# Kernel tuning notes

Hardware: AMD Instinct MI355X
Metric: run time of the kernel (lower is better)

Reference implementation:

```python
import jax, jax.numpy as jnp
import numpy as np
from jax import lax

UP = 4          # upscale_factor (pixel_shuffle factor hardcoded to 4 in ReconBlock)
OUT_CH = UP * UP * 5 * 5  # 400
MID_CH = UP * 5           # 20


def setup_inputs() -> dict:
    key = jax.random.key(0)
    ks = jax.random.split(key, 5)
    B, A, H, W = 2, 5, 96, 96
    pic = jax.random.uniform(ks[0], (B, A, A, H, W), dtype=jnp.float32)
    w1 = jax.random.normal(ks[1], (OUT_CH, 1, 5, 5, 9, 9), dtype=jnp.float32) * 0.02
    b1 = jnp.zeros((OUT_CH,), jnp.float32)
    w2a = jax.random.normal(ks[2], (MID_CH, 1, 3, 3, 5, 5), dtype=jnp.float32) * 0.02
    b2a = jnp.zeros((MID_CH,), jnp.float32)
    w2b = jax.random.normal(ks[3], (OUT_CH, MID_CH, 3, 3, 5, 5), dtype=jnp.float32) * 0.02
    b2b = jnp.zeros((OUT_CH,), jnp.float32)
    return {"pic": pic, "w1": w1, "b1": b1, "w2a": w2a, "b2a": b2a,
            "w2b": w2b, "b2b": b2b}


def _conv4d(x, w):
    # x: [B, Cin, A1, A2, H, W], w: [Cout, Cin, k1, k2, k3, k4], VALID, stride 1
    return lax.conv_general_dilated(x, w, window_strides=(1, 1, 1, 1),
                                    padding='VALID')


def _bias(b):
    return b[None, :, None, None, None, None]


def reference(pic, w1, b1, w2a, b2a, w2b, b2b):
    B, A1, A2, H, W = pic.shape
    # Padder: pad H,W by 4 each side with value 0.5
    padded = jnp.full((B, A1, A2, H + 8, W + 8), 0.5, dtype=pic.dtype)
    padded = padded.at[:, :, :, 4:-4, 4:-4].set(pic)
    x = padded[:, None]  # [B,1,A1,A2,H+8,W+8]

    # DimBlock_1: single 4D conv (5,5,9,9); ReLU defined but never applied
    p1 = _conv4d(x, w1) + _bias(b1)              # [B,400,1,1,H,W]

    # DimBlock_2: two 4D convs (3,3,5,5) with ReLU
    buf = jax.nn.relu(_conv4d(x, w2a) + _bias(b2a))   # [B,20,3,3,H+4,W+4]
    p2 = jax.nn.relu(_conv4d(buf, w2b) + _bias(b2b))  # [B,400,1,1,H,W]

    # BottleNeck
    mid = (p1 + p2) / 2                           # [B,400,1,1,H,W]

    # ReconBlock: take angular position (0,0), pixel_shuffle(4), split 25 -> 5x5
    y = mid[:, :, 0, 0]                           # [B,400,H,W]
    Bc, C, Hh, Ww = y.shape
    r = 4
    y = y.reshape(Bc, 25, r, r, Hh, Ww)
    y = y.transpose(0, 1, 4, 2, 5, 3).reshape(Bc, 25, Hh * r, Ww * r)
    return y.reshape(Bc, 5, 5, Hh * r, Ww * r)
```

## Files before the change

### kernel.cpp

```cpp
#include <hip/hip_runtime.h>
#include <hip/hip_bf16.h>


typedef __attribute__((ext_vector_type(8))) unsigned short ushort8;
typedef __attribute__((ext_vector_type(8))) __bf16 bf16x8;
typedef __attribute__((ext_vector_type(4))) float f32x4;

#define NB 2
#define HSLOT 576
#define HBUF (4 * HSLOT * 8)
#define WST 14336
#define NWA (6 * 25 * 7 * 4 * 64 * 8)
#define NWB (81 * 7 * 4 * 64 * 8)

static __device__ __forceinline__ unsigned short f2bf(float f) {
    __hip_bfloat16 h = __float2bfloat16(f);
    return *reinterpret_cast<unsigned short*>(&h);
}
static __device__ __forceinline__ void gload16(const unsigned short* g, unsigned short* l) {
    __builtin_amdgcn_global_load_lds(
        (const __attribute__((address_space(1))) unsigned int*)(const void*)g,
        (__attribute__((address_space(3))) unsigned int*)(void*)l, 16, 0, 0);
}

#define MFMA16(A0, A1, A2, A3, B0, B1, B2, B3)                                          \
    {                                                                                   \
        __builtin_amdgcn_s_setprio(1);                                                  \
        acc[0][0] = __builtin_amdgcn_mfma_f32_16x16x32_bf16(A0, B0, acc[0][0], 0, 0, 0);\
        acc[0][1] = __builtin_amdgcn_mfma_f32_16x16x32_bf16(A0, B1, acc[0][1], 0, 0, 0);\
        acc[0][2] = __builtin_amdgcn_mfma_f32_16x16x32_bf16(A0, B2, acc[0][2], 0, 0, 0);\
        acc[0][3] = __builtin_amdgcn_mfma_f32_16x16x32_bf16(A0, B3, acc[0][3], 0, 0, 0);\
        acc[1][0] = __builtin_amdgcn_mfma_f32_16x16x32_bf16(A1, B0, acc[1][0], 0, 0, 0);\
        acc[1][1] = __builtin_amdgcn_mfma_f32_16x16x32_bf16(A1, B1, acc[1][1], 0, 0, 0);\
        acc[1][2] = __builtin_amdgcn_mfma_f32_16x16x32_bf16(A1, B2, acc[1][2], 0, 0, 0);\
        acc[1][3] = __builtin_amdgcn_mfma_f32_16x16x32_bf16(A1, B3, acc[1][3], 0, 0, 0);\
        acc[2][0] = __builtin_amdgcn_mfma_f32_16x16x32_bf16(A2, B0, acc[2][0], 0, 0, 0);\
        acc[2][1] = __builtin_amdgcn_mfma_f32_16x16x32_bf16(A2, B1, acc[2][1], 0, 0, 0);\
        acc[2][2] = __builtin_amdgcn_mfma_f32_16x16x32_bf16(A2, B2, acc[2][2], 0, 0, 0);\
        acc[2][3] = __builtin_amdgcn_mfma_f32_16x16x32_bf16(A2, B3, acc[2][3], 0, 0, 0);\
        acc[3][0] = __builtin_amdgcn_mfma_f32_16x16x32_bf16(A3, B0, acc[3][0], 0, 0, 0);\
        acc[3][1] = __builtin_amdgcn_mfma_f32_16x16x32_bf16(A3, B1, acc[3][1], 0, 0, 0);\
        acc[3][2] = __builtin_amdgcn_mfma_f32_16x16x32_bf16(A3, B2, acc[3][2], 0, 0, 0);\
        acc[3][3] = __builtin_amdgcn_mfma_f32_16x16x32_bf16(A3, B3, acc[3][3], 0, 0, 0);\
        __builtin_amdgcn_s_setprio(0);                                                  \
    }

__global__ __launch_bounds__(256) void pad_kernel(const float* __restrict__ pic,
                                                  unsigned short* __restrict__ Pn) {
    int idx = blockIdx.x * 256 + threadIdx.x;
    if (idx >= NB * 104 * 104) return;
    int x = idx % 104;
    int y = (idx / 104) % 104;
    int b = idx / (104 * 104);
    unsigned short vals[32];
    bool inter = (y >= 4 && y < 100 && x >= 4 && x < 100);
#pragma unroll
    for (int c = 0; c < 25; ++c) {
        float v = inter ? pic[((b * 25 + c) * 96 + (y - 4)) * 96 + (x - 4)] : 0.5f;
        vals[c] = f2bf(v);
    }
#pragma unroll
    for (int c = 25; c < 32; ++c) vals[c] = 0;
    ushort8* dst = (ushort8*)(Pn + idx * 32);
#pragma unroll
    for (int j = 0; j < 4; ++j) dst[j] = *(ushort8*)&vals[j * 8];
}

__global__ __launch_bounds__(256) void prep_w_kernel(const float* __restrict__ w2b,
                                                     const float* __restrict__ w1,
                                                     unsigned short* __restrict__ Wp) {
    int idx = blockIdx.x * 256 + threadIdx.x;
    if (idx < NWA) {
        int e = idx & 7, lane = (idx >> 3) & 63, n = (idx >> 9) & 3;
        int r = idx >> 11;
        int ocb = r % 7; r /= 7;
        int tap = r % 25; int cc = r / 25;
        int oc = ocb * 64 + n * 16 + (lane & 15);
        int k  = cc * 32 + (lane >> 4) * 8 + e;
        float v = 0.f;
        if (oc < 400 && k < 180) {
            int mc = k % 20, uv = k / 20;
            v = w2b[oc * 4500 + (mc * 9 + uv) * 25 + tap];
        }
        Wp[idx] = f2bf(v);
    } else {
        int kx = idx - NWA;
        if (kx >= NWB) return;
        int e = kx & 7, lane = (kx >> 3) & 63, n = (kx >> 9) & 3;
        int r = kx >> 11;
        int ocb = r % 7; int tp = r / 7;
        int dy, dx;
        if (tp < 45) { dy = tp / 5; dx = tp % 5; }
        else { int u = tp - 45; dy = u >> 2; dx = 5 + (u & 3); }
        int oc = ocb * 64 + n * 16 + (lane & 15);
        int c  = (lane >> 4) * 8 + e;
        float v = (oc < 400 && c < 25) ? w1[oc * 2025 + c * 81 + (dy * 9 + dx)] : 0.f;
        Wp[NWA + kx] = f2bf(v);
    }
}

__global__ __launch_bounds__(256) void conv2a_mfma_kernel(
    const unsigned short* __restrict__ Pn, const float* __restrict__ w2a,
    const float* __restrict__ b2a, unsigned short* __restrict__ Bn) {
    __shared__ __align__(16) unsigned short sWc[25 * 2048];
    __shared__ __align__(16) unsigned short sHalo[4 * 448 * 8];

    const int tid  = threadIdx.x;
    const int lane = tid & 63, w = tid >> 6;
    const int l15  = lane & 15, lhi = lane >> 4;
    const int gx0  = blockIdx.x;
    const int b    = gx0 / 52, t52 = gx0 % 52;
    const int ty0  = (t52 >> 2) * 8;
    const int tx0  = (t52 & 3) * 32;
    const int ocB  = blockIdx.y;

    {
        int oc = ocB * 64 + w * 16 + (lane & 15);
        int kb = (lane >> 4) * 8;
        int uv = oc / 20;
        int mc = oc - uv * 20;
        int u = uv / 3, v = uv - (uv / 3) * 3;
        const float* wb[8];
#pragma unroll
        for (int e = 0; e < 8; ++e) {
            int k  = kb + e;
            int c1 = k / 5, c2 = k - (k / 5) * 5;
            int da1 = c1 - u, da2 = c2 - v;
            bool valid = (oc < 180) && ((unsigned)da1 < 3u) && ((unsigned)da2 < 3u);
            wb[e] = valid ? (w2a + mc * 225 + (da1 * 3 + da2) * 25) : (const float*)0;
        }
#pragma unroll
        for (int tap = 0; tap < 25; ++tap) {
            unsigned short fr[8];
#pragma unroll
            for (int e = 0; e < 8; ++e) fr[e] = wb[e] ? f2bf(wb[e][tap]) : (unsigned short)0;
            *(ushort8*)&sWc[tap * 2048 + tid * 8] = *(ushort8*)fr;
        }
    }

    for (int L2 = 0; L2 < 7; ++L2) {
        int p = L2 * 64 + lane;
        if (p >= 432) p = 0;
        int hy = (p * 58255) >> 21, hx = p - hy * 36;
        int gy = ty0 + hy; gy = gy > 103 ? 103 : gy;
        int gx = tx0 + hx; gx = gx > 103 ? 103 : gx;
        gload16(Pn + ((size_t)((b * 104 + gy) * 104 + gx)) * 32 + w * 8,
                &sHalo[(w * 448 + L2 * 64) * 8]);
    }
    float bs[4];
#pragma unroll
    for (int n = 0; n < 4; ++n) {
        int oc = ocB * 64 + n * 16 + l15;
        bs[n] = (oc < 180) ? b2a[oc % 20] : 0.f;
    }
    __syncthreads();

    const unsigned short* hb = &sHalo[(lhi * 448 + w * 72 + l15) * 8];
    const unsigned short* wc = &sWc[lane * 8];

    f32x4 acc[4][4] = {};
    bf16x8 a0 = *(const bf16x8*)(hb), a1 = *(const bf16x8*)(hb + 128);
    bf16x8 a2 = *(const bf16x8*)(hb + 288), a3 = *(const bf16x8*)(hb + 416);
    bf16x8 c0 = *(const bf16x8*)(wc), c1 = *(const bf16x8*)(wc + 512);
    bf16x8 c2 = *(const bf16x8*)(wc + 1024), c3 = *(const bf16x8*)(wc + 1536);
    bf16x8 q0, q1, q2, q3, n0, n1, n2, n3;
#pragma unroll
    for (int t = 0; t < 25; ++t) {
        if (t < 24) {
            const int u = (((t + 1) / 5) * 36 + ((t + 1) % 5)) * 8;
            q0 = *(const bf16x8*)(hb + u);
            q1 = *(const bf16x8*)(hb + u + 128);
            q2 = *(const bf16x8*)(hb + u + 288);
            q3 = *(const bf16x8*)(hb + u + 416);
            const unsigned short* wn = wc + (t + 1) * 2048;
            n0 = *(const bf16x8*)(wn);
            n1 = *(const bf16x8*)(wn + 512);
            n2 = *(const bf16x8*)(wn + 1024);
            n3 = *(const bf16x8*)(wn + 1536);
        }
        MFMA16(a0, a1, a2, a3, c0, c1, c2, c3);
        if (t < 24) { a0 = q0; a1 = q1; a2 = q2; a3 = q3;
                      c0 = n0; c1 = n1; c2 = n2; c3 = n3; }
    }

#pragma unroll
    for (int n = 0; n < 4; ++n) {
        int oc = ocB * 64 + n * 16 + l15;
#pragma unroll
        for (int m = 0; m < 4; ++m) {
            int y = ty0 + w * 2 + (m >> 1);
            if (y >= 100) continue;
            int x0 = tx0 + (m & 1) * 16 + lhi * 4;
#pragma unroll
            for (int i = 0; i < 4; ++i) {
                int x = x0 + i;
                if (x >= 100) continue;
                Bn[((size_t)((b * 100 + y) * 100 + x)) * 192 + oc] =
                    f2bf(fmaxf(acc[m][n][i] + bs[n], 0.f));
            }
        }
    }
}

__global__ __launch_bounds__(256, 2) void conv_mfma_kernel(
    const unsigned short* __restrict__ Pn, const unsigned short* __restrict__ Bn,
    const unsigned short* __restrict__ Wp, const float* __restrict__ b1,
    const float* __restrict__ b2b, float* __restrict__ out) {
    __shared__ __align__(16) unsigned short sHalo[2 * HBUF];

    const int tid  = threadIdx.x;
    const int lane = tid & 63, w = tid >> 6;
    const int l15  = lane & 15, lhi = lane >> 4;
    const int ocB  = blockIdx.y;
    const int pb   = blockIdx.x;
    const int b    = pb / 36;
    const int t36  = pb % 36;
    const int ty0  = (t36 / 3) * 8;
    const int tx0  = (t36 % 3) * 32;

    const int vA = (lhi * HSLOT + w * 72 + l15) * 8;

    auto stageA = [&](int cc, int par) {
        unsigned short* dst0 = &sHalo[par * HBUF + w * HSLOT * 8];
        for (int L2 = 0; L2 < 7; ++L2) {
            int p = L2 * 64 + lane;
            if (p >= 432) p = 0;
            int hy = (p * 58255) >> 21, hx = p - hy * 36;
            gload16(Bn + ((size_t)((b * 100 + ty0 + hy) * 100 + tx0 + hx)) * 192 +
                        cc * 32 + w * 8,
                    dst0 + L2 * 512);
        }
    };
    auto stageB = [&](int seg, int par) {
        int cx = tx0 + (seg == 7 ? 5 : 0);
        unsigned short* dst0 = &sHalo[par * HBUF + w * HSLOT * 8];
        for (int L2 = 0; L2 < 9; ++L2) {
            int p = L2 * 64 + lane;
            int hy = (p * 58255) >> 21, hx = p - hy * 36;
            int gx = cx + hx;
            gx = gx > 103 ? 103 : gx;
            gload16(Pn + ((size_t)((b * 104 + ty0 + hy) * 104 + gx)) * 32 + w * 8,
                    dst0 + L2 * 512);
        }
    };

    float bb2[4], bb1[4];
#pragma unroll
    for (int n = 0; n < 4; ++n) {
        int oc  = ocB * 64 + n * 16 + l15;
        int occ = oc < 400 ? oc : 399;
        bb2[n] = b2b[occ];
        bb1[n] = b1[occ];
    }

    const unsigned short* wq = Wp + ocB * 2048 + lane * 8;
    bf16x8 c0 = *(const bf16x8*)(wq);
    bf16x8 c1 = *(const bf16x8*)(wq + 512);
    bf16x8 c2 = *(const bf16x8*)(wq + 1024);
    bf16x8 c3 = *(const bf16x8*)(wq + 1536);
    stageA(0, 0);
    __syncthreads();

    f32x4 acc[4][4] = {};
    bf16x8 a0, a1, a2, a3, q0, q1, q2, q3, n0, n1, n2, n3;

    for (int cc = 0; cc < 6; ++cc) {
        const unsigned short* hb = &sHalo[(cc & 1) * HBUF + vA];
        a0 = *(const bf16x8*)(hb);
        a1 = *(const bf16x8*)(hb + 128);
        a2 = *(const bf16x8*)(hb + 288);
        a3 = *(const bf16x8*)(hb + 416);
        if (cc < 5) stageA(cc + 1, (cc + 1) & 1);
        else        stageB(6, 0);
#pragma unroll
        for (int t = 0; t < 25; ++t) {
            wq += WST;
            n0 = *(const bf16x8*)(wq);
            n1 = *(const bf16x8*)(wq + 512);
            n2 = *(const bf16x8*)(wq + 1024);
            n3 = *(const bf16x8*)(wq + 1536);
            if (t < 24) {
                const int u = (((t + 1) / 5) * 36 + ((t + 1) % 5)) * 8;
                q0 = *(const bf16x8*)(hb + u);
                q1 = *(const bf16x8*)(hb + u + 128);
                q2 = *(const bf16x8*)(hb + u + 288);
                q3 = *(const bf16x8*)(hb + u + 416);
            }
            MFMA16(a0, a1, a2, a3, c0, c1, c2, c3);
            c0 = n0; c1 = n1; c2 = n2; c3 = n3;
            if (t < 24) { a0 = q0; a1 = q1; a2 = q2; a3 = q3; }
        }
        if (cc == 5) {
#pragma unroll
            for (int m = 0; m < 4; ++m)
#pragma unroll
                for (int n = 0; n < 4; ++n)
#pragma unroll
                    for (int i = 0; i < 4; ++i)
                        acc[m][n][i] = fmaxf(acc[m][n][i] + bb2[n], 0.f);
        }
        asm volatile("s_waitcnt vmcnt(4)" ::: "memory");
        asm volatile("s_barrier" ::: "memory");
    }

    {
        const unsigned short* hb = &sHalo[vA];
        a0 = *(const bf16x8*)(hb);
        a1 = *(const bf16x8*)(hb + 128);
        a2 = *(const bf16x8*)(hb + 288);
        a3 = *(const bf16x8*)(hb + 416);
        stageB(7, 1);
#pragma unroll
        for (int t = 0; t < 45; ++t) {
            wq += WST;
            n0 = *(const bf16x8*)(wq);
            n1 = *(const bf16x8*)(wq + 512);
            n2 = *(const bf16x8*)(wq + 1024);
            n3 = *(const bf16x8*)(wq + 1536);
            if (t < 44) {
                const int u = (((t + 1) / 5) * 36 + ((t + 1) % 5)) * 8;
                q0 = *(const bf16x8*)(hb + u);
                q1 = *(const bf16x8*)(hb + u + 128);
                q2 = *(const bf16x8*)(hb + u + 288);
                q3 = *(const bf16x8*)(hb + u + 416);
            }
            MFMA16(a0, a1, a2, a3, c0, c1, c2, c3);
            c0 = n0; c1 = n1; c2 = n2; c3 = n3;
            if (t < 44) { a0 = q0; a1 = q1; a2 = q2; a3 = q3; }
        }
        asm volatile("s_waitcnt vmcnt(4)" ::: "memory");
        asm volatile("s_barrier" ::: "memory");
    }

    {
        const unsigned short* hb = &sHalo[HBUF + vA];
        a0 = *(const bf16x8*)(hb);
        a1 = *(const bf16x8*)(hb + 128);
        a2 = *(const bf16x8*)(hb + 288);
        a3 = *(const bf16x8*)(hb + 416);
#pragma unroll
        for (int t = 0; t < 36; ++t) {
            if (t < 35) {
                wq += WST;
                n0 = *(const bf16x8*)(wq);
                n1 = *(const bf16x8*)(wq + 512);
                n2 = *(const bf16x8*)(wq + 1024);
                n3 = *(const bf16x8*)(wq + 1536);
                const int u = (((t + 1) / 4) * 36 + ((t + 1) % 4)) * 8;
                q0 = *(const bf16x8*)(hb + u);
                q1 = *(const bf16x8*)(hb + u + 128);
                q2 = *(const bf16x8*)(hb + u + 288);
                q3 = *(const bf16x8*)(hb + u + 416);
            }
            MFMA16(a0, a1, a2, a3, c0, c1, c2, c3);
            if (t < 35) { a0 = q0; a1 = q1; a2 = q2; a3 = q3;
                          c0 = n0; c1 = n1; c2 = n2; c3 = n3; }
        }
    }

#pragma unroll
    for (int n = 0; n < 4; ++n) {
        int oc = ocB * 64 + n * 16 + l15;
        if (oc >= 400) continue;
        float bv = bb1[n];
        int c25 = oc >> 4, r1 = (oc >> 2) & 3, r2 = oc & 3;
#pragma unroll
        for (int m = 0; m < 4; ++m) {
            int y  = ty0 + w * 2 + (m >> 1);
            int x0 = tx0 + (m & 1) * 16 + lhi * 4;
#pragma unroll
            for (int i = 0; i < 4; ++i) {
                out[((size_t)(b * 25 + c25) * 384 + y * 4 + r1) * 384 + (x0 + i) * 4 + r2] =
                    (acc[m][n][i] + bv) * 0.5f;
            }
        }
    }
}

extern "C" void kernel_launch(void* const* d_in, const int* in_sizes, int n_in,
                              void* d_out, int out_size, void* d_ws, size_t ws_size,
                              hipStream_t stream) {
    const float* pic = (const float*)d_in[0];
    const float* w1  = (const float*)d_in[1];
    const float* b1  = (const float*)d_in[2];
    const float* w2a = (const float*)d_in[3];
    const float* b2a = (const float*)d_in[4];
    const float* w2b = (const float*)d_in[5];
    const float* b2b = (const float*)d_in[6];
    float* out = (float*)d_out;

    char* ws = (char*)d_ws;
    unsigned short* Pn = (unsigned short*)(ws);
    unsigned short* Bn = (unsigned short*)(ws + 1384448);
    unsigned short* Wp = (unsigned short*)(ws + 9064448);

    pad_kernel<<<(NB * 104 * 104 + 255) / 256, 256, 0, stream>>>(pic, Pn);
    prep_w_kernel<<<(NWA + NWB + 255) / 256, 256, 0, stream>>>(w2b, w1, Wp);
    conv2a_mfma_kernel<<<dim3(104, 3), 256, 0, stream>>>(Pn, w2a, b2a, Bn);
    conv_mfma_kernel<<<dim3(72, 7), 256, 0, stream>>>(Pn, Bn, Wp, b1, b2b, out);
}
```

Baseline: 160.0 us.

## Split conv taps across wave pairs with LDS reduction and larger per-wave M tile

Restructures the main conv kernel so each wave computes an 8x4 MFMA tile (doubling the rows per wave) while pairs of waves split the K-loop taps in half, reducing partial sums through an LDS exchange buffer. This halves the weight-fragment loads per MFMA and increases reuse of B fragments. In exchange it drops double-buffered halo staging and software prefetch, adds full barriers between stages, and doubles accumulator registers, which may reduce occupancy. The weight prep kernel is also vectorised to write 8 bf16 values per thread.

```diff
diff --git a/kernel.cpp b/kernel.cpp
--- a/kernel.cpp
+++ b/kernel.cpp
@@ -8,7 +8,6 @@
 
 #define NB 2
 #define HSLOT 576
-#define HBUF (4 * HSLOT * 8)
 #define WST 14336
 #define NWA (6 * 25 * 7 * 4 * 64 * 8)
 #define NWB (81 * 7 * 4 * 64 * 8)
@@ -21,6 +20,72 @@
     __builtin_amdgcn_global_load_lds(
         (const __attribute__((address_space(1))) unsigned int*)(const void*)g,
         (__attribute__((address_space(3))) unsigned int*)(void*)l, 16, 0, 0);
+}
+
+__global__ __launch_bounds__(256) void pad_kernel(const float* __restrict__ pic,
+                                                  unsigned short* __restrict__ Pn) {
+    int idx = blockIdx.x * 256 + threadIdx.x;
+    if (idx >= NB * 104 * 104) return;
+    int x = idx % 104;
+    int y = (idx / 104) % 104;
+    int b = idx / (104 * 104);
+    unsigned short vals[32];
+    bool inter = (y >= 4 && y < 100 && x >= 4 && x < 100);
+#pragma unroll
+    for (int c = 0; c < 25; ++c) {
+        float v = inter ? pic[((b * 25 + c) * 96 + (y - 4)) * 96 + (x - 4)] : 0.5f;
+        vals[c] = f2bf(v);
+    }
+#pragma unroll
+    for (int c = 25; c < 32; ++c) vals[c] = 0;
+    ushort8* dst = (ushort8*)(Pn + idx * 32);
+#pragma unroll
+    for (int j = 0; j < 4; ++j) dst[j] = *(ushort8*)&vals[j * 8];
+}
+
+__global__ __launch_bounds__(256) void prep_w_kernel(const float* __restrict__ w2b,
+                                                     const float* __restrict__ w1,
+                                                     unsigned short* __restrict__ Wp) {
+    int t = blockIdx.x * 256 + threadIdx.x;
+    const int NW8 = (NWA + NWB) / 8;
+    if (t >= NW8) return;
+    int base = t * 8;
+    unsigned short v8[8];
+    if (base < NWA) {
+        int lane = (base >> 3) & 63, n = (base >> 9) & 3;
+        int r = base >> 11;
+        int ocb = r % 7; r /= 7;
+        int tap = r % 25; int cc = r / 25;
+        int oc = ocb * 64 + n * 16 + (lane & 15);
+        int kb = cc * 32 + (lane >> 4) * 8;
+#pragma unroll
+        for (int e = 0; e < 8; ++e) {
+            int k = kb + e;
+            float v = 0.f;
+            if (oc < 400 && k < 180) {
+                int mc = k % 20, uv = k / 20;
+                v = w2b[oc * 4500 + (mc * 9 + uv) * 25 + tap];
+            }
+            v8[e] = f2bf(v);
+        }
+    } else {
+        int kx = base - NWA;
+        int lane = (kx >> 3) & 63, n = (kx >> 9) & 3;
+        int r = kx >> 11;
+        int ocb = r % 7; int tp = r / 7;
+        int dy, dx;
+        if (tp < 45) { dy = tp / 5; dx = tp % 5; }
+        else { int u = tp - 45; dy = u >> 2; dx = 5 + (u & 3); }
+        int oc = ocb * 64 + n * 16 + (lane & 15);
+        int cb = (lane >> 4) * 8;
+#pragma unroll
+        for (int e = 0; e < 8; ++e) {
+            int c = cb + e;
+            float v = (oc < 400 && c < 25) ? w1[oc * 2025 + c * 81 + (dy * 9 + dx)] : 0.f;
+            v8[e] = f2bf(v);
+        }
+    }
+    *(ushort8*)(Wp + base) = *(ushort8*)v8;
 }
 
 #define MFMA16(A0, A1, A2, A3, B0, B1, B2, B3)                                          \
@@ -45,60 +110,6 @@
         __builtin_amdgcn_s_setprio(0);                                                  \
     }
 
-__global__ __launch_bounds__(256) void pad_kernel(const float* __restrict__ pic,
-                                                  unsigned short* __restrict__ Pn) {
-    int idx = blockIdx.x * 256 + threadIdx.x;
-    if (idx >= NB * 104 * 104) return;
-    int x = idx % 104;
-    int y = (idx / 104) % 104;
-    int b = idx / (104 * 104);
-    unsigned short vals[32];
-    bool inter = (y >= 4 && y < 100 && x >= 4 && x < 100);
-#pragma unroll
-    for (int c = 0; c < 25; ++c) {
-        float v = inter ? pic[((b * 25 + c) * 96 + (y - 4)) * 96 + (x - 4)] : 0.5f;
-        vals[c] = f2bf(v);
-    }
-#pragma unroll
-    for (int c = 25; c < 32; ++c) vals[c] = 0;
-    ushort8* dst = (ushort8*)(Pn + idx * 32);
-#pragma unroll
-    for (int j = 0; j < 4; ++j) dst[j] = *(ushort8*)&vals[j * 8];
-}
-
-__global__ __launch_bounds__(256) void prep_w_kernel(const float* __restrict__ w2b,
-                                                     const float* __restrict__ w1,
-                                                     unsigned short* __restrict__ Wp) {
-    int idx = blockIdx.x * 256 + threadIdx.x;
-    if (idx < NWA) {
-        int e = idx & 7, lane = (idx >> 3) & 63, n = (idx >> 9) & 3;
-        int r = idx >> 11;
-        int ocb = r % 7; r /= 7;
-        int tap = r % 25; int cc = r / 25;
-        int oc = ocb * 64 + n * 16 + (lane & 15);
-        int k  = cc * 32 + (lane >> 4) * 8 + e;
-        float v = 0.f;
-        if (oc < 400 && k < 180) {
-            int mc = k % 20, uv = k / 20;
-            v = w2b[oc * 4500 + (mc * 9 + uv) * 25 + tap];
-        }
-        Wp[idx] = f2bf(v);
-    } else {
-        int kx = idx - NWA;
-        if (kx >= NWB) return;
-        int e = kx & 7, lane = (kx >> 3) & 63, n = (kx >> 9) & 3;
-        int r = kx >> 11;
-        int ocb = r % 7; int tp = r / 7;
-        int dy, dx;
-        if (tp < 45) { dy = tp / 5; dx = tp % 5; }
-        else { int u = tp - 45; dy = u >> 2; dx = 5 + (u & 3); }
-        int oc = ocb * 64 + n * 16 + (lane & 15);
-        int c  = (lane >> 4) * 8 + e;
-        float v = (oc < 400 && c < 25) ? w1[oc * 2025 + c * 81 + (dy * 9 + dx)] : 0.f;
-        Wp[NWA + kx] = f2bf(v);
-    }
-}
-
 __global__ __launch_bounds__(256) void conv2a_mfma_kernel(
     const unsigned short* __restrict__ Pn, const float* __restrict__ w2a,
     const float* __restrict__ b2a, unsigned short* __restrict__ Bn) {
@@ -206,41 +217,42 @@
     const unsigned short* __restrict__ Pn, const unsigned short* __restrict__ Bn,
     const unsigned short* __restrict__ Wp, const float* __restrict__ b1,
     const float* __restrict__ b2b, float* __restrict__ out) {
-    __shared__ __align__(16) unsigned short sHalo[2 * HBUF];
-
-    const int tid  = threadIdx.x;
-    const int lane = tid & 63, w = tid >> 6;
-    const int l15  = lane & 15, lhi = lane >> 4;
-    const int ocB  = blockIdx.y;
-    const int pb   = blockIdx.x;
-    const int b    = pb / 36;
-    const int t36  = pb % 36;
-    const int ty0  = (t36 / 3) * 8;
-    const int tx0  = (t36 % 3) * 32;
-
-    const int vA = (lhi * HSLOT + w * 72 + l15) * 8;
-
-    auto stageA = [&](int cc, int par) {
-        unsigned short* dst0 = &sHalo[par * HBUF + w * HSLOT * 8];
+    __shared__ __align__(16) unsigned short sHalo[4 * HSLOT * 8];
+    __shared__ __align__(16) float sExch[2][4096];
+
+    const int tid   = threadIdx.x;
+    const int lane  = tid & 63, w = tid >> 6;
+    const int l15   = lane & 15, lhi = lane >> 4;
+    const int pairI = w >> 1;
+    const int kh    = w & 1;
+    const int ocB   = blockIdx.y;
+    const int pb    = blockIdx.x;
+    const int b     = pb / 36;
+    const int t36   = pb % 36;
+    const int ty0   = (t36 / 3) * 8;
+    const int tx0   = (t36 % 3) * 32;
+
+    const int vA = (lhi * HSLOT + pairI * 144 + l15) * 8;
+
+    auto stageA = [&](int cc) {
         for (int L2 = 0; L2 < 7; ++L2) {
             int p = L2 * 64 + lane;
             if (p >= 432) p = 0;
             int hy = (p * 58255) >> 21, hx = p - hy * 36;
             gload16(Bn + ((size_t)((b * 100 + ty0 + hy) * 100 + tx0 + hx)) * 192 +
                         cc * 32 + w * 8,
-                    dst0 + L2 * 512);
-        }
-    };
-    auto stageB = [&](int seg, int par) {
+                    &sHalo[(w * HSLOT + L2 * 64) * 8]);
+        }
+    };
+    auto stageB = [&](int seg) {
         int cx = tx0 + (seg == 7 ? 5 : 0);
-        unsigned short* dst0 = &sHalo[par * HBUF + w * HSLOT * 8];
         for (int L2 = 0; L2 < 9; ++L2) {
             int p = L2 * 64 + lane;
             int hy = (p * 58255) >> 21, hx = p - hy * 36;
             int gx = cx + hx;
             gx = gx > 103 ? 103 : gx;
             gload16(Pn + ((size_t)((b * 104 + ty0 + hy) * 104 + gx)) * 32 + w * 8,
-                    dst0 + L2 * 512);
+                    &sHalo[(w * HSLOT + L2 * 64) * 8]);
         }
     };
 
@@ -253,125 +265,125 @@
         bb1[n] = b1[occ];
     }
 
-    const unsigned short* wq = Wp + ocB * 2048 + lane * 8;
-    bf16x8 c0 = *(const bf16x8*)(wq);
-    bf16x8 c1 = *(const bf16x8*)(wq + 512);
-    bf16x8 c2 = *(const bf16x8*)(wq + 1024);
-    bf16x8 c3 = *(const bf16x8*)(wq + 1536);
-    stageA(0, 0);
+    f32x4 acc[8][4] = {};
+
+    constexpr int AOFF[8] = {0, 128, 288, 416, 576, 704, 864, 992};
+
+    auto tap = [&](const unsigned short* ha, const unsigned short* wp) {
+        bf16x8 af[8], cf[4];
+#pragma unroll
+        for (int m = 0; m < 8; ++m) af[m] = *(const bf16x8*)(ha + AOFF[m]);
+#pragma unroll
+        for (int n = 0; n < 4; ++n) cf[n] = *(const bf16x8*)(wp + n * 512);
+        __builtin_amdgcn_s_setprio(1);
+#pragma unroll
+        for (int m = 0; m < 8; ++m)
+#pragma unroll
+            for (int n = 0; n < 4; ++n)
+                acc[m][n] = __builtin_amdgcn_mfma_f32_16x16x32_bf16(af[m], cf[n],
+                                                                    acc[m][n], 0, 0, 0);
+        __builtin_amdgcn_s_setprio(0);
+    };
+
+    auto runseg = [&](int sbase, int kb, int nt, bool b2m) {
+        const unsigned short* wp = Wp + (size_t)(sbase + kb) * WST + ocB * 2048 + lane * 8;
+#pragma unroll
+        for (int t = 0; t < nt; ++t) {
+            int k = kb + t;
+            int hoff = b2m ? (((k >> 2) * 36 + (k & 3)) * 8)
+                           : (((k / 5) * 36 + (k % 5)) * 8);
+            tap(&sHalo[vA + hoff], wp);
+            wp += WST;
+        }
+    };
+
+    auto exwrite = [&](int h) {
+#pragma unroll
+        for (int mm = 0; mm < 4; ++mm)
+#pragma unroll
+            for (int n = 0; n < 4; ++n)
+#pragma unroll
+                for (int i = 0; i < 4; ++i)
+                    sExch[pairI][(mm * 16 + n * 4 + i) * 64 + lane] = acc[h * 4 + mm][n][i];
+    };
+    auto exread = [&](int h) {
+#pragma unroll
+        for (int mm = 0; mm < 4; ++mm)
+#pragma unroll
+            for (int n = 0; n < 4; ++n)
+#pragma unroll
+                for (int i = 0; i < 4; ++i)
+                    acc[h * 4 + mm][n][i] += sExch[pairI][(mm * 16 + n * 4 + i) * 64 + lane];
+    };
+
+    stageA(0);
     __syncthreads();
-
-    f32x4 acc[4][4] = {};
-    bf16x8 a0, a1, a2, a3, q0, q1, q2, q3, n0, n1, n2, n3;
-
     for (int cc = 0; cc < 6; ++cc) {
-        const unsigned short* hb = &sHalo[(cc & 1) * HBUF + vA];
-        a0 = *(const bf16x8*)(hb);
-        a1 = *(const bf16x8*)(hb + 128);
-        a2 = *(const bf16x8*)(hb + 288);
-        a3 = *(const bf16x8*)(hb + 416);
-        if (cc < 5) stageA(cc + 1, (cc + 1) & 1);
-        else        stageB(6, 0);
-#pragma unroll
-        for (int t = 0; t < 25; ++t) {
-            wq += WST;
-            n0 = *(const bf16x8*)(wq);
-            n1 = *(const bf16x8*)(wq + 512);
-            n2 = *(const bf16x8*)(wq + 1024);
-            n3 = *(const bf16x8*)(wq + 1536);
-            if (t < 24) {
-                const int u = (((t + 1) / 5) * 36 + ((t + 1) % 5)) * 8;
-                q0 = *(const bf16x8*)(hb + u);
-                q1 = *(const bf16x8*)(hb + u + 128);
-                q2 = *(const bf16x8*)(hb + u + 288);
-                q3 = *(const bf16x8*)(hb + u + 416);
-            }
-            MFMA16(a0, a1, a2, a3, c0, c1, c2, c3);
-            c0 = n0; c1 = n1; c2 = n2; c3 = n3;
-            if (t < 24) { a0 = q0; a1 = q1; a2 = q2; a3 = q3; }
-        }
-        if (cc == 5) {
-#pragma unroll
-            for (int m = 0; m < 4; ++m)
-#pragma unroll
-                for (int n = 0; n < 4; ++n)
-#pragma unroll
-                    for (int i = 0; i < 4; ++i)
-                        acc[m][n][i] = fmaxf(acc[m][n][i] + bb2[n], 0.f);
-        }
-        asm volatile("s_waitcnt vmcnt(4)" ::: "memory");
-        asm volatile("s_barrier" ::: "memory");
-    }
-
-    {
-        const unsigned short* hb = &sHalo[vA];
-        a0 = *(const bf16x8*)(hb);
-        a1 = *(const bf16x8*)(hb + 128);
-        a2 = *(const bf16x8*)(hb + 288);
-        a3 = *(const bf16x8*)(hb + 416);
-        stageB(7, 1);
-#pragma unroll
-        for (int t = 0; t < 45; ++t) {
-            wq += WST;
-            n0 = *(const bf16x8*)(wq);
-            n1 = *(const bf16x8*)(wq + 512);
-            n2 = *(const bf16x8*)(wq + 1024);
-            n3 = *(const bf16x8*)(wq + 1536);
-            if (t < 44) {
-                const int u = (((t + 1) / 5) * 36 + ((t + 1) % 5)) * 8;
-                q0 = *(const bf16x8*)(hb + u);
-                q1 = *(const bf16x8*)(hb + u + 128);
-                q2 = *(const bf16x8*)(hb + u + 288);
-                q3 = *(const bf16x8*)(hb + u + 416);
-            }
-            MFMA16(a0, a1, a2, a3, c0, c1, c2, c3);
-            c0 = n0; c1 = n1; c2 = n2; c3 = n3;
-            if (t < 44) { a0 = q0; a1 = q1; a2 = q2; a3 = q3; }
-        }
-        asm volatile("s_waitcnt vmcnt(4)" ::: "memory");
-        asm volatile("s_barrier" ::: "memory");
-    }
-
-    {
-        const unsigned short* hb = &sHalo[HBUF + vA];
-        a0 = *(const bf16x8*)(hb);
-        a1 = *(const bf16x8*)(hb + 128);
-        a2 = *(const bf16x8*)(hb + 288);
-        a3 = *(const bf16x8*)(hb + 416);
-#pragma unroll
-        for (int t = 0; t < 36; ++t) {
-            if (t < 35) {
-                wq += WST;
-                n0 = *(const bf16x8*)(wq);
-                n1 = *(const bf16x8*)(wq + 512);
-                n2 = *(const bf16x8*)(wq + 1024);
-                n3 = *(const bf16x8*)(wq + 1536);
-                const int u = (((t + 1) / 4) * 36 + ((t + 1) % 4)) * 8;
-                q0 = *(const bf16x8*)(hb + u);
-                q1 = *(const bf16x8*)(hb + u + 128);
-                q2 = *(const bf16x8*)(hb + u + 288);
-                q3 = *(const bf16x8*)(hb + u + 416);
-            }
-            MFMA16(a0, a1, a2, a3, c0, c1, c2, c3);
-            if (t < 35) { a0 = q0; a1 = q1; a2 = q2; a3 = q3;
-                          c0 = n0; c1 = n1; c2 = n2; c3 = n3; }
-        }
-    }
-
-#pragma unroll
-    for (int n = 0; n < 4; ++n) {
-        int oc = ocB * 64 + n * 16 + l15;
-        if (oc >= 400) continue;
-        float bv = bb1[n];
-        int c25 = oc >> 4, r1 = (oc >> 2) & 3, r2 = oc & 3;
-#pragma unroll
-        for (int m = 0; m < 4; ++m) {
-            int y  = ty0 + w * 2 + (m >> 1);
-            int x0 = tx0 + (m & 1) * 16 + lhi * 4;
-#pragma unroll
-            for (int i = 0; i < 4; ++i) {
-                out[((size_t)(b * 25 + c25) * 384 + y * 4 + r1) * 384 + (x0 + i) * 4 + r2] =
-                    (acc[m][n][i] + bv) * 0.5f;
+        if (kh) runseg(cc * 25, 13, 12, false);
+        else    runseg(cc * 25,  0, 13, false);
+        __syncthreads();
+        if (cc < 5) {
+            stageA(cc + 1);
+            __syncthreads();
+        }
+    }
+
+    stageB(6);
+#pragma unroll
+    for (int h = 0; h < 2; ++h) {
+        if (!kh) exwrite(h);
+        __syncthreads();
+        if (kh) exread(h);
+        __syncthreads();
+    }
+    if (kh) {
+#pragma unroll
+        for (int m = 0; m < 8; ++m)
+#pragma unroll
+            for (int n = 0; n < 4; ++n)
+#pragma unroll
+                for (int i = 0; i < 4; ++i)
+                    acc[m][n][i] = fmaxf(acc[m][n][i] + bb2[n], 0.f);
+    } else {
+#pragma unroll
+        for (int m = 0; m < 8; ++m)
+#pragma unroll
+            for (int n = 0; n < 4; ++n)
+                acc[m][n] = f32x4{0.f, 0.f, 0.f, 0.f};
+    }
+
+    if (kh) runseg(150, 23, 22, false);
+    else    runseg(150,  0, 23, false);
+    __syncthreads();
+    stageB(7);
+    __syncthreads();
+
+    if (kh) runseg(195, 18, 18, true);
+    else    runseg(195,  0, 18, true);
+
+#pragma unroll
+    for (int h = 0; h < 2; ++h) {
+        if (!kh) exwrite(h);
+        __syncthreads();
+        if (kh) exread(h);
+        if (h == 0) __syncthreads();
+    }
+    if (kh) {
+#pragma unroll
+        for (int n = 0; n < 4; ++n) {
+            int oc = ocB * 64 + n * 16 + l15;
+            if (oc >= 400) continue;
+            float bv = bb1[n];
+            int c25 = oc >> 4, r1 = (oc >> 2) & 3, r2 = oc & 3;
+#pragma unroll
+            for (int m = 0; m < 8; ++m) {
+                int y  = ty0 + pairI * 4 + (m >> 1);
+                int x0 = tx0 + (m & 1) * 16 + lhi * 4;
+#pragma unroll
+                for (int i = 0; i < 4; ++i) {
+                    out[((size_t)(b * 25 + c25) * 384 + y * 4 + r1) * 384 + (x0 + i) * 4 + r2] =
+                        (acc[m][n][i] + bv) * 0.5f;
+                }
             }
         }
     }
@@ -395,7 +407,7 @@
     unsigned short* Wp = (unsigned short*)(ws + 9064448);
 
     pad_kernel<<<(NB * 104 * 104 + 255) / 256, 256, 0, stream>>>(pic, Pn);
-    prep_w_kernel<<<(NWA + NWB + 255) / 256, 256, 0, stream>>>(w2b, w1, Wp);
+    prep_w_kernel<<<(((NWA + NWB) / 8) + 255) / 256, 256, 0, stream>>>(w2b, w1, Wp);
     conv2a_mfma_kernel<<<dim3(104, 3), 256, 0, stream>>>(Pn, w2a, b2a, Bn);
     conv_mfma_kernel<<<dim3(72, 7), 256, 0, stream>>>(Pn, Bn, Wp, b1, b2b, out);
 }
```

Result: slower. 191.0 us (+19.4%).

## Fuse pad and weight-prep kernels; precompute conv2a weights and split its channel blocks

Applied to the files above, without the earlier changes.

Merges the pad and weight-packing kernels into one launch whose block ranges handle the input padding, the w2b and w1 packing, and a new pre-packed conv2a weight buffer. The w2b and w1 packing now goes through a shared-memory transpose so global reads and writes are coalesced. conv2a no longer rebuilds its weights in LDS in every block; it reads the pre-packed weights from global memory and uses 32 output channels per block over twice as many blocks. This saves a launch and the redundant per-block weight construction, but the conv2a weight reads now come from global or cache with no prefetch pipelining.

```diff
diff --git a/kernel.cpp b/kernel.cpp
--- a/kernel.cpp
+++ b/kernel.cpp
@@ -10,8 +10,6 @@
 #define HSLOT 576
 #define HBUF (4 * HSLOT * 8)
 #define WST 14336
-#define NWA (6 * 25 * 7 * 4 * 64 * 8)
-#define NWB (81 * 7 * 4 * 64 * 8)
 
 static __device__ __forceinline__ unsigned short f2bf(float f) {
     __hip_bfloat16 h = __float2bfloat16(f);
@@ -21,6 +19,211 @@
     __builtin_amdgcn_global_load_lds(
         (const __attribute__((address_space(1))) unsigned int*)(const void*)g,
         (__attribute__((address_space(3))) unsigned int*)(void*)l, 16, 0, 0);
+}
+
+__global__ __launch_bounds__(256) void prep_fused_kernel(
+    const float* __restrict__ pic, const float* __restrict__ w1,
+    const float* __restrict__ w2a, const float* __restrict__ w2b,
+    unsigned short* __restrict__ Pn, unsigned short* __restrict__ Wp,
+    unsigned short* __restrict__ Wc2) {
+    __shared__ unsigned short sT[28544];
+    const int blk = blockIdx.x;
+    const int tid = threadIdx.x;
+
+    if (blk < 85) {
+        int idx = blk * 256 + tid;
+        if (idx >= NB * 104 * 104) return;
+        int x = idx % 104;
+        int y = (idx / 104) % 104;
+        int b = idx / (104 * 104);
+        unsigned short vals[32];
+        bool inter = (y >= 4 && y < 100 && x >= 4 && x < 100);
+#pragma unroll
+        for (int c = 0; c < 25; ++c) {
+            float v = inter ? pic[((b * 25 + c) * 96 + (y - 4)) * 96 + (x - 4)] : 0.5f;
+            vals[c] = f2bf(v);
+        }
+#pragma unroll
+        for (int c = 25; c < 32; ++c) vals[c] = 0;
+        ushort8* dst = (ushort8*)(Pn + idx * 32);
+#pragma unroll
+        for (int j = 0; j < 4; ++j) dst[j] = *(ushort8*)&vals[j * 8];
+    } else if (blk < 127) {
+        int b2 = blk - 85;
+        int ocB = b2 % 7, cc = b2 / 7;
+        for (int n32 = 0; n32 < 2; ++n32) {
+            for (int j = 0; j < 4; ++j) {
+                int p  = tid * 4 + j;
+                int gl = p >> 5, ol = p & 31;
+                int oc = ocB * 64 + n32 * 32 + ol;
+                int gp = cc * 32 + gl;
+                const float* src = nullptr;
+                if (oc < 400 && gp < 180) {
+                    int mc = gp % 20, uv = gp / 20;
+                    src = w2b + oc * 4500 + (mc * 9 + uv) * 25;
+                }
+#pragma unroll
+                for (int tap = 0; tap < 25; ++tap)
+                    sT[(gl * 25 + tap) * 33 + ol] = src ? f2bf(src[tap]) : (unsigned short)0;
+            }
+            __syncthreads();
+            for (int i = 0; i < 13; ++i) {
+                int sid = i * 256 + tid;
+                if (sid < 3200) {
+                    int tap = sid >> 7;
+                    int r   = sid & 127;
+                    int nb = r >> 6, lane = r & 63;
+                    int kq = lane >> 4;
+                    int olw = nb * 16 + (lane & 15);
+                    unsigned short v8[8];
+#pragma unroll
+                    for (int e = 0; e < 8; ++e)
+                        v8[e] = sT[((kq * 8 + e) * 25 + tap) * 33 + olw];
+                    size_t d = (size_t)(cc * 25 + tap) * WST + ocB * 2048 +
+                               (n32 * 2 + nb) * 512 + lane * 8;
+                    *(ushort8*)(Wp + d) = *(ushort8*)v8;
+                }
+            }
+            __syncthreads();
+        }
+    } else if (blk < 148) {
+        int b3 = blk - 127;
+        int ocB = b3 % 7, tt = b3 / 7;
+        for (int n32 = 0; n32 < 2; ++n32) {
+            for (int j = 0; j < 4; ++j) {
+                int p  = tid * 4 + j;
+                int cl = p >> 5, ol = p & 31;
+                int oc = ocB * 64 + n32 * 32 + ol;
+                const float* src = (oc < 400 && cl < 25)
+                                       ? (w1 + oc * 2025 + cl * 81 + tt * 27) : nullptr;
+#pragma unroll
+                for (int tl = 0; tl < 27; ++tl)
+                    sT[(cl * 27 + tl) * 33 + ol] = src ? f2bf(src[tl]) : (unsigned short)0;
+            }
+            __syncthreads();
+            for (int i = 0; i < 14; ++i) {
+                int sid = i * 256 + tid;
+                if (sid < 3456) {
+                    int tl = sid >> 7;
+                    int r  = sid & 127;
+                    int nb = r >> 6, lane = r & 63;
+                    int kq = lane >> 4;
+                    int olw = nb * 16 + (lane & 15);
+                    unsigned short v8[8];
+#pragma unroll
+                    for (int e = 0; e < 8; ++e)
+                        v8[e] = sT[((kq * 8 + e) * 27 + tl) * 33 + olw];
+                    int tap_lin = tt * 27 + tl;
+                    int dy = tap_lin / 9, dx = tap_lin % 9;
+                    int tp = (dx < 5) ? (dy * 5 + dx) : (45 + dy * 4 + (dx - 5));
+                    size_t d = (size_t)(150 + tp) * WST + ocB * 2048 +
+                               (n32 * 2 + nb) * 512 + lane * 8;
+                    *(ushort8*)(Wp + d) = *(ushort8*)v8;
+                }
+            }
+            __syncthreads();
+        }
+    } else if (blk < 154) {
+        int ocB2 = blk - 148;
+        if (tid < 128) {
+            int lane = tid & 63;
+            int oc = ocB2 * 32 + (tid >> 6) * 16 + (lane & 15);
+            int kb = (lane >> 4) * 8;
+            int uv = oc / 20, mc = oc % 20;
+            int u = uv / 3, v = uv % 3;
+            const float* wb[8];
+#pragma unroll
+            for (int e = 0; e < 8; ++e) {
+                int k  = kb + e;
+                int c1 = k / 5, c2 = k % 5;
+                int da1 = c1 - u, da2 = c2 - v;
+                bool valid = (oc < 180) && ((unsigned)da1 < 3u) && ((unsigned)da2 < 3u);
+                wb[e] = valid ? (w2a + mc * 225 + (da1 * 3 + da2) * 25) : (const float*)0;
+            }
+            for (int tap = 0; tap < 25; ++tap) {
+                unsigned short fr[8];
+#pragma unroll
+                for (int e = 0; e < 8; ++e) fr[e] = wb[e] ? f2bf(wb[e][tap]) : (unsigned short)0;
+                *(ushort8*)(Wc2 + ((size_t)(ocB2 * 25 + tap) * 128 + tid) * 8) = *(ushort8*)fr;
+            }
+        }
+    }
+}
+
+__global__ __launch_bounds__(256) void conv2a_mfma_kernel(
+    const unsigned short* __restrict__ Pn, const unsigned short* __restrict__ Wc2,
+    const float* __restrict__ b2a, unsigned short* __restrict__ Bn) {
+    __shared__ __align__(16) unsigned short sHalo[4 * 448 * 8];
+
+    const int tid  = threadIdx.x;
+    const int lane = tid & 63, w = tid >> 6;
+    const int l15  = lane & 15, lhi = lane >> 4;
+    const int gx0  = blockIdx.x;
+    const int b    = gx0 / 52, t52 = gx0 % 52;
+    const int ty0  = (t52 >> 2) * 8;
+    const int tx0  = (t52 & 3) * 32;
+    const int ocB  = blockIdx.y;
+
+    for (int L2 = 0; L2 < 7; ++L2) {
+        int p = L2 * 64 + lane;
+        if (p >= 432) p = 0;
+        int hy = (p * 58255) >> 21, hx = p - hy * 36;
+        int gy = ty0 + hy; gy = gy > 103 ? 103 : gy;
+        int gx = tx0 + hx; gx = gx > 103 ? 103 : gx;
+        gload16(Pn + ((size_t)((b * 104 + gy) * 104 + gx)) * 32 + w * 8,
+                &sHalo[(w * 448 + L2 * 64) * 8]);
+    }
+    float bs[2];
+#pragma unroll
+    for (int n = 0; n < 2; ++n) {
+        int oc = ocB * 32 + n * 16 + l15;
+        bs[n] = (oc < 180) ? b2a[oc % 20] : 0.f;
+    }
+    __syncthreads();
+
+    const unsigned short* hb = &sHalo[(lhi * 448 + w * 72 + l15) * 8];
+    const unsigned short* wq = Wc2 + (size_t)ocB * 25600 + lane * 8;
+
+    f32x4 acc[4][2] = {};
+#pragma unroll
+    for (int t = 0; t < 25; ++t) {
+        const int u = ((t / 5) * 36 + (t % 5)) * 8;
+        bf16x8 a0 = *(const bf16x8*)(hb + u);
+        bf16x8 a1 = *(const bf16x8*)(hb + u + 128);
+        bf16x8 a2 = *(const bf16x8*)(hb + u + 288);
+        bf16x8 a3 = *(const bf16x8*)(hb + u + 416);
+        bf16x8 c0 = *(const bf16x8*)(wq);
+        bf16x8 c1 = *(const bf16x8*)(wq + 512);
+        __builtin_amdgcn_s_setprio(1);
+        acc[0][0] = __builtin_amdgcn_mfma_f32_16x16x32_bf16(a0, c0, acc[0][0], 0, 0, 0);
+        acc[0][1] = __builtin_amdgcn_mfma_f32_16x16x32_bf16(a0, c1, acc[0][1], 0, 0, 0);
+        acc[1][0] = __builtin_amdgcn_mfma_f32_16x16x32_bf16(a1, c0, acc[1][0], 0, 0, 0);
+        acc[1][1] = __builtin_amdgcn_mfma_f32_16x16x32_bf16(a1, c1, acc[1][1], 0, 0, 0);
+        acc[2][0] = __builtin_amdgcn_mfma_f32_16x16x32_bf16(a2, c0, acc[2][0], 0, 0, 0);
+        acc[2][1] = __builtin_amdgcn_mfma_f32_16x16x32_bf16(a2, c1, acc[2][1], 0, 0, 0);
+        acc[3][0] = __builtin_amdgcn_mfma_f32_16x16x32_bf16(a3, c0, acc[3][0], 0, 0, 0);
+        acc[3][1] = __builtin_amdgcn_mfma_f32_16x16x32_bf16(a3, c1, acc[3][1], 0, 0, 0);
+        __builtin_amdgcn_s_setprio(0);
+        wq += 1024;
+    }
+
+#pragma unroll
+    for (int n = 0; n < 2; ++n) {
+        int oc = ocB * 32 + n * 16 + l15;
+#pragma unroll
+        for (int m = 0; m < 4; ++m) {
+            int y = ty0 + w * 2 + (m >> 1);
+            if (y >= 100) continue;
+            int x0 = tx0 + (m & 1) * 16 + lhi * 4;
+#pragma unroll
+            for (int i = 0; i < 4; ++i) {
+                int x = x0 + i;
+                if (x >= 100) continue;
+                Bn[((size_t)((b * 100 + y) * 100 + x)) * 192 + oc] =
+                    f2bf(fmaxf(acc[m][n][i] + bs[n], 0.f));
+            }
+        }
+    }
 }
 
 #define MFMA16(A0, A1, A2, A3, B0, B1, B2, B3)                                          \
@@ -45,163 +248,6 @@
         __builtin_amdgcn_s_setprio(0);                                                  \
     }
 
-__global__ __launch_bounds__(256) void pad_kernel(const float* __restrict__ pic,
-                                                  unsigned short* __restrict__ Pn) {
-    int idx = blockIdx.x * 256 + threadIdx.x;
-    if (idx >= NB * 104 * 104) return;
-    int x = idx % 104;
-    int y = (idx / 104) % 104;
-    int b = idx / (104 * 104);
-    unsigned short vals[32];
-    bool inter = (y >= 4 && y < 100 && x >= 4 && x < 100);
-#pragma unroll
-    for (int c = 0; c < 25; ++c) {
-        float v = inter ? pic[((b * 25 + c) * 96 + (y - 4)) * 96 + (x - 4)] : 0.5f;
-        vals[c] = f2bf(v);
-    }
-#pragma unroll
-    for (int c = 25; c < 32; ++c) vals[c] = 0;
-    ushort8* dst = (ushort8*)(Pn + idx * 32);
-#pragma unroll
-    for (int j = 0; j < 4; ++j) dst[j] = *(ushort8*)&vals[j * 8];
-}
-
-__global__ __launch_bounds__(256) void prep_w_kernel(const float* __restrict__ w2b,
-                                                     const float* __restrict__ w1,
-                                                     unsigned short* __restrict__ Wp) {
-    int idx = blockIdx.x * 256 + threadIdx.x;
-    if (idx < NWA) {
-        int e = idx & 7, lane = (idx >> 3) & 63, n = (idx >> 9) & 3;
-        int r = idx >> 11;
-        int ocb = r % 7; r /= 7;
-        int tap = r % 25; int cc = r / 25;
-        int oc = ocb * 64 + n * 16 + (lane & 15);
-        int k  = cc * 32 + (lane >> 4) * 8 + e;
-        float v = 0.f;
-        if (oc < 400 && k < 180) {
-            int mc = k % 20, uv = k / 20;
-            v = w2b[oc * 4500 + (mc * 9 + uv) * 25 + tap];
-        }
-        Wp[idx] = f2bf(v);
-    } else {
-        int kx = idx - NWA;
-        if (kx >= NWB) return;
-        int e = kx & 7, lane = (kx >> 3) & 63, n = (kx >> 9) & 3;
-        int r = kx >> 11;
-        int ocb = r % 7; int tp = r / 7;
-        int dy, dx;
-        if (tp < 45) { dy = tp / 5; dx = tp % 5; }
-        else { int u = tp - 45; dy = u >> 2; dx = 5 + (u & 3); }
-        int oc = ocb * 64 + n * 16 + (lane & 15);
-        int c  = (lane >> 4) * 8 + e;
-        float v = (oc < 400 && c < 25) ? w1[oc * 2025 + c * 81 + (dy * 9 + dx)] : 0.f;
-        Wp[NWA + kx] = f2bf(v);
-    }
-}
-
-__global__ __launch_bounds__(256) void conv2a_mfma_kernel(
-    const unsigned short* __restrict__ Pn, const float* __restrict__ w2a,
-    const float* __restrict__ b2a, unsigned short* __restrict__ Bn) {
-    __shared__ __align__(16) unsigned short sWc[25 * 2048];
-    __shared__ __align__(16) unsigned short sHalo[4 * 448 * 8];
-
-    const int tid  = threadIdx.x;
-    const int lane = tid & 63, w = tid >> 6;
-    const int l15  = lane & 15, lhi = lane >> 4;
-    const int gx0  = blockIdx.x;
-    const int b    = gx0 / 52, t52 = gx0 % 52;
-    const int ty0  = (t52 >> 2) * 8;
-    const int tx0  = (t52 & 3) * 32;
-    const int ocB  = blockIdx.y;
-
-    {
-        int oc = ocB * 64 + w * 16 + (lane & 15);
-        int kb = (lane >> 4) * 8;
-        int uv = oc / 20;
-        int mc = oc - uv * 20;
-        int u = uv / 3, v = uv - (uv / 3) * 3;
-        const float* wb[8];
-#pragma unroll
-        for (int e = 0; e < 8; ++e) {
-            int k  = kb + e;
-            int c1 = k / 5, c2 = k - (k / 5) * 5;
-            int da1 = c1 - u, da2 = c2 - v;
-            bool valid = (oc < 180) && ((unsigned)da1 < 3u) && ((unsigned)da2 < 3u);
-            wb[e] = valid ? (w2a + mc * 225 + (da1 * 3 + da2) * 25) : (const float*)0;
-        }
-#pragma unroll
-        for (int tap = 0; tap < 25; ++tap) {
-            unsigned short fr[8];
-#pragma unroll
-            for (int e = 0; e < 8; ++e) fr[e] = wb[e] ? f2bf(wb[e][tap]) : (unsigned short)0;
-            *(ushort8*)&sWc[tap * 2048 + tid * 8] = *(ushort8*)fr;
-        }
-    }
-
-    for (int L2 = 0; L2 < 7; ++L2) {
-        int p = L2 * 64 + lane;
-        if (p >= 432) p = 0;
-        int hy = (p * 58255) >> 21, hx = p - hy * 36;
-        int gy = ty0 + hy; gy = gy > 103 ? 103 : gy;
-        int gx = tx0 + hx; gx = gx > 103 ? 103 : gx;
-        gload16(Pn + ((size_t)((b * 104 + gy) * 104 + gx)) * 32 + w * 8,
-                &sHalo[(w * 448 + L2 * 64) * 8]);
-    }
-    float bs[4];
-#pragma unroll
-    for (int n = 0; n < 4; ++n) {
-        int oc = ocB * 64 + n * 16 + l15;
-        bs[n] = (oc < 180) ? b2a[oc % 20] : 0.f;
-    }
-    __syncthreads();
-
-    const unsigned short* hb = &sHalo[(lhi * 448 + w * 72 + l15) * 8];
-    const unsigned short* wc = &sWc[lane * 8];
-
-    f32x4 acc[4][4] = {};
-    bf16x8 a0 = *(const bf16x8*)(hb), a1 = *(const bf16x8*)(hb + 128);
-    bf16x8 a2 = *(const bf16x8*)(hb + 288), a3 = *(const bf16x8*)(hb + 416);
-    bf16x8 c0 = *(const bf16x8*)(wc), c1 = *(const bf16x8*)(wc + 512);
-    bf16x8 c2 = *(const bf16x8*)(wc + 1024), c3 = *(const bf16x8*)(wc + 1536);
-    bf16x8 q0, q1, q2, q3, n0, n1, n2, n3;
-#pragma unroll
-    for (int t = 0; t < 25; ++t) {
-        if (t < 24) {
-            const int u = (((t + 1) / 5) * 36 + ((t + 1) % 5)) * 8;
-            q0 = *(const bf16x8*)(hb + u);
-            q1 = *(const bf16x8*)(hb + u + 128);
-            q2 = *(const bf16x8*)(hb + u + 288);
-            q3 = *(const bf16x8*)(hb + u + 416);
-            const unsigned short* wn = wc + (t + 1) * 2048;
-            n0 = *(const bf16x8*)(wn);
-            n1 = *(const bf16x8*)(wn + 512);
-            n2 = *(const bf16x8*)(wn + 1024);
-            n3 = *(const bf16x8*)(wn + 1536);
-        }
-        MFMA16(a0, a1, a2, a3, c0, c1, c2, c3);
-        if (t < 24) { a0 = q0; a1 = q1; a2 = q2; a3 = q3;
-                      c0 = n0; c1 = n1; c2 = n2; c3 = n3; }
-    }
-
-#pragma unroll
-    for (int n = 0; n < 4; ++n) {
-        int oc = ocB * 64 + n * 16 + l15;
-#pragma unroll
-        for (int m = 0; m < 4; ++m) {
-            int y = ty0 + w * 2 + (m >> 1);
-            if (y >= 100) continue;
-            int x0 = tx0 + (m & 1) * 16 + lhi * 4;
-#pragma unroll
-            for (int i = 0; i < 4; ++i) {
-                int x = x0 + i;
-                if (x >= 100) continue;
-                Bn[((size_t)((b * 100 + y) * 100 + x)) * 192 + oc] =
-                    f2bf(fmaxf(acc[m][n][i] + bs[n], 0.f));
-            }
-        }
-    }
-}
-
 __global__ __launch_bounds__(256, 2) void conv_mfma_kernel(
     const unsigned short* __restrict__ Pn, const unsigned short* __restrict__ Bn,
     const unsigned short* __restrict__ Wp, const float* __restrict__ b1,
@@ -390,12 +436,12 @@
     float* out = (float*)d_out;
 
     char* ws = (char*)d_ws;
-    unsigned short* Pn = (unsigned short*)(ws);
-    unsigned short* Bn = (unsigned short*)(ws + 1384448);
-    unsigned short* Wp = (unsigned short*)(ws + 9064448);
-
-    pad_kernel<<<(NB * 104 * 104 + 255) / 256, 256, 0, stream>>>(pic, Pn);
-    prep_w_kernel<<<(NWA + NWB + 255) / 256, 256, 0, stream>>>(w2b, w1, Wp);
-    conv2a_mfma_kernel<<<dim3(104, 3), 256, 0, stream>>>(Pn, w2a, b2a, Bn);
+    unsigned short* Pn  = (unsigned short*)(ws);
+    unsigned short* Bn  = (unsigned short*)(ws + 1384448);
+    unsigned short* Wp  = (unsigned short*)(ws + 9064448);
+    unsigned short* Wc2 = (unsigned short*)(ws + 15687680);
+
+    prep_fused_kernel<<<154, 256, 0, stream>>>(pic, w1, w2a, w2b, Pn, Wp, Wc2);
+    conv2a_mfma_kernel<<<dim3(104, 6), 256, 0, stream>>>(Pn, Wc2, b2a, Bn);
     conv_mfma_kernel<<<dim3(72, 7), 256, 0, stream>>>(Pn, Bn, Wp, b1, b2b, out);
 }
```

Result: faster. 149.2 us (-6.7%).
